# Performance work log

Hardware: AMD Instinct MI355X
Metric: run time of the kernel (lower is better)

Reference implementation:

```python
import jax, jax.numpy as jnp
import numpy as np

N_REVIEWS = 1_000_000
N_USERS = 100_000
N_ITEMS = 50_000
D = 64  # per-entity embedding dim; input_dim = 3*D = 192
D_OUT = 64


def setup_inputs() -> dict:
    key = jax.random.key(0)
    k1, k2, k3, k4, k5, k6, k7, k8 = jax.random.split(key, 8)
    review_vecs = jax.random.normal(k1, (N_REVIEWS, D), dtype=jnp.float32)
    user_vecs = jax.random.normal(k2, (N_USERS, D), dtype=jnp.float32)
    item_vecs = jax.random.normal(k3, (N_ITEMS, D), dtype=jnp.float32)
    W = jax.random.normal(k4, (3 * D, D_OUT), dtype=jnp.float32) * (1.0 / np.sqrt(3 * D))
    review_user_adj = jax.random.randint(k5, (N_REVIEWS,), 0, N_USERS, dtype=jnp.int32)
    review_item_adj = jax.random.randint(k6, (N_REVIEWS,), 0, N_ITEMS, dtype=jnp.int32)
    # tf.random_shuffle on the transposed gather shuffles the feature axis;
    # modeled as fixed permutations for determinism.
    perm_u = jax.random.permutation(k7, D).astype(jnp.int32)
    perm_i = jax.random.permutation(k8, D).astype(jnp.int32)
    return {
        "review_vecs": review_vecs,
        "user_vecs": user_vecs,
        "item_vecs": item_vecs,
        "W": W,
        "review_user_adj": review_user_adj,
        "review_item_adj": review_item_adj,
        "perm_u": perm_u,
        "perm_i": perm_i,
    }


def reference(review_vecs, user_vecs, item_vecs, W,
              review_user_adj, review_item_adj, perm_u, perm_i):
    # dropout = 0.0 -> identity
    ri = item_vecs[review_item_adj][:, perm_i]   # [N_reviews, D] gather + feature shuffle
    ru = user_vecs[review_user_adj][:, perm_u]   # [N_reviews, D]
    concat = jnp.concatenate([review_vecs, ru, ri], axis=1)  # [N_reviews, 3D]
    out = concat @ W                              # [N_reviews, D_OUT]
    return jax.nn.relu(out)
```

## Files before the change

kernel.cpp:

```cpp
#include <hip/hip_runtime.h>
#include <hip/hip_bf16.h>


#define DIMS 64
#define K3 192
#define MTILE 64
#define LDST 208

typedef float f32x4 __attribute__((ext_vector_type(4)));
typedef short s16x8 __attribute__((ext_vector_type(8)));
typedef __bf16 bf16x8 __attribute__((ext_vector_type(8)));

__device__ __forceinline__ short f2bf(float f) {
    union { float f; unsigned int u; } v; v.f = f;
    unsigned int u = v.u;
    u += 0x7fffu + ((u >> 16) & 1u);
    return (short)(u >> 16);
}

__global__ void prep_WT(const float* __restrict__ W,
                        const int* __restrict__ perm_u,
                        const int* __restrict__ perm_i,
                        short* __restrict__ WT) {
    const int t = threadIdx.x;
    #pragma unroll 4
    for (int i = 0; i < 48; ++i) {
        int e = t + i * 256;
        int k = e >> 6;
        int n = e & 63;
        float w = W[e];
        int dk;
        if (k < 64)       dk = k;
        else if (k < 128) dk = 64 + perm_u[k - 64];
        else              dk = 128 + perm_i[k - 128];
        WT[n * K3 + dk] = f2bf(w);
    }
}

__device__ __forceinline__ void stage16(const float* __restrict__ src, short* dst) {
    const float4* s4 = (const float4*)src;
    float4 a = s4[0], b = s4[1], c = s4[2], d = s4[3];
    s16x8 lo, hi;
    lo[0] = f2bf(a.x); lo[1] = f2bf(a.y); lo[2] = f2bf(a.z); lo[3] = f2bf(a.w);
    lo[4] = f2bf(b.x); lo[5] = f2bf(b.y); lo[6] = f2bf(b.z); lo[7] = f2bf(b.w);
    hi[0] = f2bf(c.x); hi[1] = f2bf(c.y); hi[2] = f2bf(c.z); hi[3] = f2bf(c.w);
    hi[4] = f2bf(d.x); hi[5] = f2bf(d.y); hi[6] = f2bf(d.z); hi[7] = f2bf(d.w);
    ((s16x8*)dst)[0] = lo;
    ((s16x8*)dst)[1] = hi;
}

__global__ __launch_bounds__(256) void concat_agg_kernel(
        const float* __restrict__ review,
        const float* __restrict__ user,
        const float* __restrict__ item,
        const int* __restrict__ uadj,
        const int* __restrict__ iadj,
        const short* __restrict__ WT,
        float* __restrict__ out,
        int n_reviews) {
    __shared__ short ldsX[MTILE * LDST];
    __shared__ short ldsW[DIMS * LDST];

    const int t = threadIdx.x;
    const int r0 = blockIdx.x * MTILE;

    #pragma unroll
    for (int i = 0; i < 6; ++i) {
        int c = t + i * 256;
        int n = c / 24;
        int k = (c - n * 24) * 8;
        s16x8 v = *(const s16x8*)(WT + c * 8);
        *(s16x8*)&ldsW[n * LDST + k] = v;
    }

    const int rloc = t >> 2;
    const int seg  = (t & 3) * 16;
    int row = r0 + rloc;
    if (row >= n_reviews) row = n_reviews - 1;

    stage16(review + (size_t)row * DIMS + seg, &ldsX[rloc * LDST + seg]);
    const int u  = uadj[row];
    stage16(user + (size_t)u * DIMS + seg, &ldsX[rloc * LDST + 64 + seg]);
    const int it = iadj[row];
    stage16(item + (size_t)it * DIMS + seg, &ldsX[rloc * LDST + 128 + seg]);

    __syncthreads();

    const int lane = t & 63;
    const int wv   = t >> 6;
    const int m    = lane & 15;
    const int q    = lane >> 4;

    const short* xa  = &ldsX[(wv * 16 + m) * LDST + q * 8];
    const short* wb0 = &ldsW[m * LDST + q * 8];

    f32x4 acc0 = {0.f,0.f,0.f,0.f}, acc1 = {0.f,0.f,0.f,0.f};
    f32x4 acc2 = {0.f,0.f,0.f,0.f}, acc3 = {0.f,0.f,0.f,0.f};

    #pragma unroll
    for (int ks = 0; ks < 6; ++ks) {
        bf16x8 a = __builtin_bit_cast(bf16x8, *(const s16x8*)(xa + ks * 32));
        bf16x8 b0 = __builtin_bit_cast(bf16x8, *(const s16x8*)(wb0 + 0 * 16 * LDST + ks * 32));
        bf16x8 b1 = __builtin_bit_cast(bf16x8, *(const s16x8*)(wb0 + 1 * 16 * LDST + ks * 32));
        bf16x8 b2 = __builtin_bit_cast(bf16x8, *(const s16x8*)(wb0 + 2 * 16 * LDST + ks * 32));
        bf16x8 b3 = __builtin_bit_cast(bf16x8, *(const s16x8*)(wb0 + 3 * 16 * LDST + ks * 32));
        acc0 = __builtin_amdgcn_mfma_f32_16x16x32_bf16(a, b0, acc0, 0, 0, 0);
        acc1 = __builtin_amdgcn_mfma_f32_16x16x32_bf16(a, b1, acc1, 0, 0, 0);
        acc2 = __builtin_amdgcn_mfma_f32_16x16x32_bf16(a, b2, acc2, 0, 0, 0);
        acc3 = __builtin_amdgcn_mfma_f32_16x16x32_bf16(a, b3, acc3, 0, 0, 0);
    }

    #pragma unroll
    for (int v = 0; v < 4; ++v) {
        const int rr = r0 + wv * 16 + q * 4 + v;
        if (rr < n_reviews) {
            float* orow = out + (size_t)rr * DIMS + m;
            orow[ 0] = fmaxf(acc0[v], 0.0f);
            orow[16] = fmaxf(acc1[v], 0.0f);
            orow[32] = fmaxf(acc2[v], 0.0f);
            orow[48] = fmaxf(acc3[v], 0.0f);
        }
    }
}

extern "C" void kernel_launch(void* const* d_in, const int* in_sizes, int n_in,
                              void* d_out, int out_size, void* d_ws, size_t ws_size,
                              hipStream_t stream) {
    (void)n_in; (void)out_size; (void)ws_size;
    const float* review = (const float*)d_in[0];
    const float* user   = (const float*)d_in[1];
    const float* item   = (const float*)d_in[2];
    const float* W      = (const float*)d_in[3];
    const int* uadj     = (const int*)d_in[4];
    const int* iadj     = (const int*)d_in[5];
    const int* perm_u   = (const int*)d_in[6];
    const int* perm_i   = (const int*)d_in[7];
    float* out = (float*)d_out;
    short* WT = (short*)d_ws;

    const int n_reviews = in_sizes[0] / DIMS;

    prep_WT<<<1, 256, 0, stream>>>(W, perm_u, perm_i, WT);

    const int grid = (n_reviews + MTILE - 1) / MTILE;
    concat_agg_kernel<<<grid, 256, 0, stream>>>(review, user, item, uadj, iadj,
                                                WT, out, n_reviews);
}
```

Measured before the change: 512.8 us.

## Make gather-GEMM kernel persistent with register prefetch of next tile

The one-shot per-tile launch becomes a persistent grid of at most 768 blocks that stride over the tiles. Each block stages the bf16 weights into LDS only once. While MFMAs run on the current tile, the review, user and item rows of the next tile are loaded into registers, and the adjacency indices for the tile after that are fetched early. The goal is to hide gather latency and remove per-block weight staging, at the cost of more registers per thread and a fixed grid size that may not match the CU count.

```diff
diff --git a/kernel.cpp b/kernel.cpp
--- a/kernel.cpp
+++ b/kernel.cpp
@@ -6,6 +6,7 @@
 #define K3 192
 #define MTILE 64
 #define LDST 208
+#define NPERSIST 768
 
 typedef float f32x4 __attribute__((ext_vector_type(4)));
 typedef short s16x8 __attribute__((ext_vector_type(8)));
@@ -37,19 +38,22 @@
     }
 }
 
-__device__ __forceinline__ void stage16(const float* __restrict__ src, short* dst) {
+__device__ __forceinline__ void load16(const float* __restrict__ src, float4* v) {
     const float4* s4 = (const float4*)src;
-    float4 a = s4[0], b = s4[1], c = s4[2], d = s4[3];
+    v[0] = s4[0]; v[1] = s4[1]; v[2] = s4[2]; v[3] = s4[3];
+}
+
+__device__ __forceinline__ void pack16(const float4* v, short* dst) {
     s16x8 lo, hi;
-    lo[0] = f2bf(a.x); lo[1] = f2bf(a.y); lo[2] = f2bf(a.z); lo[3] = f2bf(a.w);
-    lo[4] = f2bf(b.x); lo[5] = f2bf(b.y); lo[6] = f2bf(b.z); lo[7] = f2bf(b.w);
-    hi[0] = f2bf(c.x); hi[1] = f2bf(c.y); hi[2] = f2bf(c.z); hi[3] = f2bf(c.w);
-    hi[4] = f2bf(d.x); hi[5] = f2bf(d.y); hi[6] = f2bf(d.z); hi[7] = f2bf(d.w);
+    lo[0] = f2bf(v[0].x); lo[1] = f2bf(v[0].y); lo[2] = f2bf(v[0].z); lo[3] = f2bf(v[0].w);
+    lo[4] = f2bf(v[1].x); lo[5] = f2bf(v[1].y); lo[6] = f2bf(v[1].z); lo[7] = f2bf(v[1].w);
+    hi[0] = f2bf(v[2].x); hi[1] = f2bf(v[2].y); hi[2] = f2bf(v[2].z); hi[3] = f2bf(v[2].w);
+    hi[4] = f2bf(v[3].x); hi[5] = f2bf(v[3].y); hi[6] = f2bf(v[3].z); hi[7] = f2bf(v[3].w);
     ((s16x8*)dst)[0] = lo;
     ((s16x8*)dst)[1] = hi;
 }
 
-__global__ __launch_bounds__(256) void concat_agg_kernel(
+__global__ __launch_bounds__(256, 3) void concat_agg_kernel(
         const float* __restrict__ review,
         const float* __restrict__ user,
         const float* __restrict__ item,
@@ -57,69 +61,115 @@
         const int* __restrict__ iadj,
         const short* __restrict__ WT,
         float* __restrict__ out,
-        int n_reviews) {
+        int n_reviews, int ntiles) {
     __shared__ short ldsX[MTILE * LDST];
     __shared__ short ldsW[DIMS * LDST];
 
     const int t = threadIdx.x;
-    const int r0 = blockIdx.x * MTILE;
+    int tile = blockIdx.x;
+    if (tile >= ntiles) return;
 
     #pragma unroll
     for (int i = 0; i < 6; ++i) {
         int c = t + i * 256;
         int n = c / 24;
         int k = (c - n * 24) * 8;
-        s16x8 v = *(const s16x8*)(WT + c * 8);
-        *(s16x8*)&ldsW[n * LDST + k] = v;
+        *(s16x8*)&ldsW[n * LDST + k] = *(const s16x8*)(WT + c * 8);
     }
 
     const int rloc = t >> 2;
     const int seg  = (t & 3) * 16;
-    int row = r0 + rloc;
-    if (row >= n_reviews) row = n_reviews - 1;
-
-    stage16(review + (size_t)row * DIMS + seg, &ldsX[rloc * LDST + seg]);
-    const int u  = uadj[row];
-    stage16(user + (size_t)u * DIMS + seg, &ldsX[rloc * LDST + 64 + seg]);
-    const int it = iadj[row];
-    stage16(item + (size_t)it * DIMS + seg, &ldsX[rloc * LDST + 128 + seg]);
-
-    __syncthreads();
-
     const int lane = t & 63;
     const int wv   = t >> 6;
     const int m    = lane & 15;
     const int q    = lane >> 4;
+    const int nstep = gridDim.x;
 
+    short* xrow = &ldsX[rloc * LDST];
     const short* xa  = &ldsX[(wv * 16 + m) * LDST + q * 8];
     const short* wb0 = &ldsW[m * LDST + q * 8];
 
-    f32x4 acc0 = {0.f,0.f,0.f,0.f}, acc1 = {0.f,0.f,0.f,0.f};
-    f32x4 acc2 = {0.f,0.f,0.f,0.f}, acc3 = {0.f,0.f,0.f,0.f};
+    float4 qr[12];
+    {
+        int row = tile * MTILE + rloc;
+        if (row >= n_reviews) row = n_reviews - 1;
+        int u_c = uadj[row];
+        int i_c = iadj[row];
+        load16(review + (size_t)row * DIMS + seg, &qr[0]);
+        load16(user   + (size_t)u_c * DIMS + seg, &qr[4]);
+        load16(item   + (size_t)i_c * DIMS + seg, &qr[8]);
+    }
+    int u_n, i_n;
+    {
+        int tn = tile + nstep;
+        int prow = tile * MTILE + rloc;
+        if (tn < ntiles) prow = tn * MTILE + rloc;
+        if (prow >= n_reviews) prow = n_reviews - 1;
+        u_n = uadj[prow];
+        i_n = iadj[prow];
+    }
+    pack16(&qr[0], xrow + seg);
+    pack16(&qr[4], xrow + 64 + seg);
+    pack16(&qr[8], xrow + 128 + seg);
 
-    #pragma unroll
-    for (int ks = 0; ks < 6; ++ks) {
-        bf16x8 a = __builtin_bit_cast(bf16x8, *(const s16x8*)(xa + ks * 32));
-        bf16x8 b0 = __builtin_bit_cast(bf16x8, *(const s16x8*)(wb0 + 0 * 16 * LDST + ks * 32));
-        bf16x8 b1 = __builtin_bit_cast(bf16x8, *(const s16x8*)(wb0 + 1 * 16 * LDST + ks * 32));
-        bf16x8 b2 = __builtin_bit_cast(bf16x8, *(const s16x8*)(wb0 + 2 * 16 * LDST + ks * 32));
-        bf16x8 b3 = __builtin_bit_cast(bf16x8, *(const s16x8*)(wb0 + 3 * 16 * LDST + ks * 32));
-        acc0 = __builtin_amdgcn_mfma_f32_16x16x32_bf16(a, b0, acc0, 0, 0, 0);
-        acc1 = __builtin_amdgcn_mfma_f32_16x16x32_bf16(a, b1, acc1, 0, 0, 0);
-        acc2 = __builtin_amdgcn_mfma_f32_16x16x32_bf16(a, b2, acc2, 0, 0, 0);
-        acc3 = __builtin_amdgcn_mfma_f32_16x16x32_bf16(a, b3, acc3, 0, 0, 0);
-    }
+    __syncthreads();
 
-    #pragma unroll
-    for (int v = 0; v < 4; ++v) {
-        const int rr = r0 + wv * 16 + q * 4 + v;
-        if (rr < n_reviews) {
-            float* orow = out + (size_t)rr * DIMS + m;
-            orow[ 0] = fmaxf(acc0[v], 0.0f);
-            orow[16] = fmaxf(acc1[v], 0.0f);
-            orow[32] = fmaxf(acc2[v], 0.0f);
-            orow[48] = fmaxf(acc3[v], 0.0f);
+    for (;;) {
+        const int tnext = tile + nstep;
+        const bool has_next = (tnext < ntiles);
+
+        int u_nn = u_n, i_nn = i_n;
+        if (has_next) {
+            int nr = tnext * MTILE + rloc;
+            if (nr >= n_reviews) nr = n_reviews - 1;
+            load16(review + (size_t)nr * DIMS + seg, &qr[0]);
+            load16(user   + (size_t)u_n * DIMS + seg, &qr[4]);
+            load16(item   + (size_t)i_n * DIMS + seg, &qr[8]);
+            int tnn = tnext + nstep;
+            int nnr = nr;
+            if (tnn < ntiles) {
+                nnr = tnn * MTILE + rloc;
+                if (nnr >= n_reviews) nnr = n_reviews - 1;
+            }
+            u_nn = uadj[nnr];
+            i_nn = iadj[nnr];
         }
+
+        f32x4 acc0 = {0.f,0.f,0.f,0.f}, acc1 = {0.f,0.f,0.f,0.f};
+        f32x4 acc2 = {0.f,0.f,0.f,0.f}, acc3 = {0.f,0.f,0.f,0.f};
+        #pragma unroll
+        for (int ks = 0; ks < 6; ++ks) {
+            bf16x8 a  = __builtin_bit_cast(bf16x8, *(const s16x8*)(xa + ks * 32));
+            bf16x8 b0 = __builtin_bit_cast(bf16x8, *(const s16x8*)(wb0 + 0 * 16 * LDST + ks * 32));
+            bf16x8 b1 = __builtin_bit_cast(bf16x8, *(const s16x8*)(wb0 + 1 * 16 * LDST + ks * 32));
+            bf16x8 b2 = __builtin_bit_cast(bf16x8, *(const s16x8*)(wb0 + 2 * 16 * LDST + ks * 32));
+            bf16x8 b3 = __builtin_bit_cast(bf16x8, *(const s16x8*)(wb0 + 3 * 16 * LDST + ks * 32));
+            acc0 = __builtin_amdgcn_mfma_f32_16x16x32_bf16(a, b0, acc0, 0, 0, 0);
+            acc1 = __builtin_amdgcn_mfma_f32_16x16x32_bf16(a, b1, acc1, 0, 0, 0);
+            acc2 = __builtin_amdgcn_mfma_f32_16x16x32_bf16(a, b2, acc2, 0, 0, 0);
+            acc3 = __builtin_amdgcn_mfma_f32_16x16x32_bf16(a, b3, acc3, 0, 0, 0);
+        }
+
+        const int r0 = tile * MTILE;
+        #pragma unroll
+        for (int v = 0; v < 4; ++v) {
+            const int rr = r0 + wv * 16 + q * 4 + v;
+            if (rr < n_reviews) {
+                float* orow = out + (size_t)rr * DIMS + m;
+                orow[ 0] = fmaxf(acc0[v], 0.0f);
+                orow[16] = fmaxf(acc1[v], 0.0f);
+                orow[32] = fmaxf(acc2[v], 0.0f);
+                orow[48] = fmaxf(acc3[v], 0.0f);
+            }
+        }
+
+        if (!has_next) break;
+
+        pack16(&qr[0], xrow + seg);
+        pack16(&qr[4], xrow + 64 + seg);
+        pack16(&qr[8], xrow + 128 + seg);
+        u_n = u_nn; i_n = i_nn;
+        tile = tnext;
     }
 }
 
@@ -139,10 +189,11 @@
     short* WT = (short*)d_ws;
 
     const int n_reviews = in_sizes[0] / DIMS;
+    const int ntiles = (n_reviews + MTILE - 1) / MTILE;
 
     prep_WT<<<1, 256, 0, stream>>>(W, perm_u, perm_i, WT);
 
-    const int grid = (n_reviews + MTILE - 1) / MTILE;
+    const int grid = ntiles < NPERSIST ? ntiles : NPERSIST;
     concat_agg_kernel<<<grid, 256, 0, stream>>>(review, user, item, uadj, iadj,
-                                                WT, out, n_reviews);
+                                                WT, out, n_reviews, ntiles);
 }
```

After: 549.6 us. 1.07x slower.

## Load activation rows directly into MFMA A-fragments, dropping the LDS staging tile

Applied to the files above, without the earlier changes.

Each lane now loads its own review, user and item feature slices straight from global memory into registers in the layout the MFMA A operand expects, then converts them to bf16. This removes the shared-memory X tile and its write/read round trip, roughly halving LDS use per block. The launch bound now requests 5 blocks per SIMD/CU to raise occupancy. In exchange, each lane issues scattered 32-byte reads instead of contiguous 64-byte segments, which may hurt coalescing on the gathered rows, and register pressure rises.

```diff
diff --git a/kernel.cpp b/kernel.cpp
--- a/kernel.cpp
+++ b/kernel.cpp
@@ -37,19 +37,14 @@
     }
 }
 
-__device__ __forceinline__ void stage16(const float* __restrict__ src, short* dst) {
-    const float4* s4 = (const float4*)src;
-    float4 a = s4[0], b = s4[1], c = s4[2], d = s4[3];
-    s16x8 lo, hi;
-    lo[0] = f2bf(a.x); lo[1] = f2bf(a.y); lo[2] = f2bf(a.z); lo[3] = f2bf(a.w);
-    lo[4] = f2bf(b.x); lo[5] = f2bf(b.y); lo[6] = f2bf(b.z); lo[7] = f2bf(b.w);
-    hi[0] = f2bf(c.x); hi[1] = f2bf(c.y); hi[2] = f2bf(c.z); hi[3] = f2bf(c.w);
-    hi[4] = f2bf(d.x); hi[5] = f2bf(d.y); hi[6] = f2bf(d.z); hi[7] = f2bf(d.w);
-    ((s16x8*)dst)[0] = lo;
-    ((s16x8*)dst)[1] = hi;
+__device__ __forceinline__ bf16x8 pack8(float4 a, float4 b) {
+    s16x8 r;
+    r[0] = f2bf(a.x); r[1] = f2bf(a.y); r[2] = f2bf(a.z); r[3] = f2bf(a.w);
+    r[4] = f2bf(b.x); r[5] = f2bf(b.y); r[6] = f2bf(b.z); r[7] = f2bf(b.w);
+    return __builtin_bit_cast(bf16x8, r);
 }
 
-__global__ __launch_bounds__(256) void concat_agg_kernel(
+__global__ __launch_bounds__(256, 5) void concat_agg_kernel(
         const float* __restrict__ review,
         const float* __restrict__ user,
         const float* __restrict__ item,
@@ -58,40 +53,49 @@
         const short* __restrict__ WT,
         float* __restrict__ out,
         int n_reviews) {
-    __shared__ short ldsX[MTILE * LDST];
     __shared__ short ldsW[DIMS * LDST];
 
-    const int t = threadIdx.x;
-    const int r0 = blockIdx.x * MTILE;
+    const int t    = threadIdx.x;
+    const int lane = t & 63;
+    const int wv   = t >> 6;
+    const int m    = lane & 15;
+    const int q    = lane >> 4;
+    const int r0   = blockIdx.x * MTILE;
+
+    int row = r0 + wv * 16 + m;
+    if (row >= n_reviews) row = n_reviews - 1;
+
+    const int u  = uadj[row];
+    const int it = iadj[row];
 
     #pragma unroll
     for (int i = 0; i < 6; ++i) {
         int c = t + i * 256;
         int n = c / 24;
         int k = (c - n * 24) * 8;
-        s16x8 v = *(const s16x8*)(WT + c * 8);
-        *(s16x8*)&ldsW[n * LDST + k] = v;
+        *(s16x8*)&ldsW[n * LDST + k] = *(const s16x8*)(WT + c * 8);
     }
 
-    const int rloc = t >> 2;
-    const int seg  = (t & 3) * 16;
-    int row = r0 + rloc;
-    if (row >= n_reviews) row = n_reviews - 1;
-
-    stage16(review + (size_t)row * DIMS + seg, &ldsX[rloc * LDST + seg]);
-    const int u  = uadj[row];
-    stage16(user + (size_t)u * DIMS + seg, &ldsX[rloc * LDST + 64 + seg]);
-    const int it = iadj[row];
-    stage16(item + (size_t)it * DIMS + seg, &ldsX[rloc * LDST + 128 + seg]);
+    const float* rv = review + (size_t)row * DIMS + q * 8;
+    const float* uv = user   + (size_t)u   * DIMS + q * 8;
+    const float* iv = item   + (size_t)it  * DIMS + q * 8;
+    float4 x0 = ((const float4*)rv)[0],        x1 = ((const float4*)rv)[1];
+    float4 x2 = ((const float4*)(rv + 32))[0], x3 = ((const float4*)(rv + 32))[1];
+    float4 x4 = ((const float4*)uv)[0],        x5 = ((const float4*)uv)[1];
+    float4 x6 = ((const float4*)(uv + 32))[0], x7 = ((const float4*)(uv + 32))[1];
+    float4 x8 = ((const float4*)iv)[0],        x9 = ((const float4*)iv)[1];
+    float4 xa = ((const float4*)(iv + 32))[0], xb = ((const float4*)(iv + 32))[1];
 
     __syncthreads();
 
-    const int lane = t & 63;
-    const int wv   = t >> 6;
-    const int m    = lane & 15;
-    const int q    = lane >> 4;
+    bf16x8 a0 = pack8(x0, x1);
+    bf16x8 a1 = pack8(x2, x3);
+    bf16x8 a2 = pack8(x4, x5);
+    bf16x8 a3 = pack8(x6, x7);
+    bf16x8 a4 = pack8(x8, x9);
+    bf16x8 a5 = pack8(xa, xb);
+    bf16x8 afr[6] = {a0, a1, a2, a3, a4, a5};
 
-    const short* xa  = &ldsX[(wv * 16 + m) * LDST + q * 8];
     const short* wb0 = &ldsW[m * LDST + q * 8];
 
     f32x4 acc0 = {0.f,0.f,0.f,0.f}, acc1 = {0.f,0.f,0.f,0.f};
@@ -99,15 +103,14 @@
 
     #pragma unroll
     for (int ks = 0; ks < 6; ++ks) {
-        bf16x8 a = __builtin_bit_cast(bf16x8, *(const s16x8*)(xa + ks * 32));
         bf16x8 b0 = __builtin_bit_cast(bf16x8, *(const s16x8*)(wb0 + 0 * 16 * LDST + ks * 32));
         bf16x8 b1 = __builtin_bit_cast(bf16x8, *(const s16x8*)(wb0 + 1 * 16 * LDST + ks * 32));
         bf16x8 b2 = __builtin_bit_cast(bf16x8, *(const s16x8*)(wb0 + 2 * 16 * LDST + ks * 32));
         bf16x8 b3 = __builtin_bit_cast(bf16x8, *(const s16x8*)(wb0 + 3 * 16 * LDST + ks * 32));
-        acc0 = __builtin_amdgcn_mfma_f32_16x16x32_bf16(a, b0, acc0, 0, 0, 0);
-        acc1 = __builtin_amdgcn_mfma_f32_16x16x32_bf16(a, b1, acc1, 0, 0, 0);
-        acc2 = __builtin_amdgcn_mfma_f32_16x16x32_bf16(a, b2, acc2, 0, 0, 0);
-        acc3 = __builtin_amdgcn_mfma_f32_16x16x32_bf16(a, b3, acc3, 0, 0, 0);
+        acc0 = __builtin_amdgcn_mfma_f32_16x16x32_bf16(afr[ks], b0, acc0, 0, 0, 0);
+        acc1 = __builtin_amdgcn_mfma_f32_16x16x32_bf16(afr[ks], b1, acc1, 0, 0, 0);
+        acc2 = __builtin_amdgcn_mfma_f32_16x16x32_bf16(afr[ks], b2, acc2, 0, 0, 0);
+        acc3 = __builtin_amdgcn_mfma_f32_16x16x32_bf16(afr[ks], b3, acc3, 0, 0, 0);
     }
 
     #pragma unroll
```

Result: slower. 527.1 us (+2.8%).
